# Performance work log

Measured on AMD Instinct MI355X. Metric: run time of the kernel, lower is better.

The kernel has to match this reference:

```python
import jax, jax.numpy as jnp
import numpy as np

HIDDEN = 128
SIGMA_A = 15.0
FACTOR_A = 180.0 / (SIGMA_A * np.pi)  # 180/(sigma_a*pi)


def _sinusoidal_embedding(indices, d_model):
    # torch: omegas = idx.view(-1,1,1)*div_term.view(1,-1,1); cat([sin,cos],dim=2)
    # -> interleaved [sin0, cos0, sin1, cos1, ...]
    div_term = jnp.exp(jnp.arange(0, d_model, 2, dtype=jnp.float32) * (-np.log(10000.0) / d_model))
    omegas = indices[..., None] * div_term  # (*, d/2)
    emb = jnp.stack([jnp.sin(omegas), jnp.cos(omegas)], axis=-1)  # (*, d/2, 2)
    return emb.reshape(*indices.shape, d_model)


def setup_inputs() -> dict:
    key = jax.random.key(0)
    k1, k2, k3 = jax.random.split(key, 3)
    B, N = 1, 1024
    points = jax.random.normal(k1, (B, N, 3), dtype=jnp.float32)
    normals = jax.random.normal(k2, (B, N, 3), dtype=jnp.float32)
    W = jax.random.normal(k3, (HIDDEN, HIDDEN), dtype=jnp.float32) / np.sqrt(HIDDEN)
    b = jnp.zeros((HIDDEN,), dtype=jnp.float32)
    return {"points": points, "normals": normals, "W": W, "b": b}


def reference(points, normals, W, b):
    # pairwise angle between normal_i (ref) and normal_j (anc), k=1 so mean over k is a no-op
    ref = normals[:, :, None, :]   # (B,N,1,3) -> n_i
    anc = normals[:, None, :, :]   # (B,1,N,3) -> n_j
    cross = jnp.cross(ref, anc)                    # (B,N,N,3)
    sin_v = jnp.linalg.norm(cross, axis=-1)        # (B,N,N)
    cos_v = jnp.sum(ref * anc, axis=-1)            # (B,N,N)
    angles = jnp.arctan2(sin_v, cos_v)
    a_indices = angles * FACTOR_A
    a_emb = _sinusoidal_embedding(a_indices, HIDDEN)  # (B,N,N,HIDDEN)
    a_emb = jax.lax.stop_gradient(a_emb)  # torch: no_grad + detach
    return a_emb @ W.T + b                # nn.Linear
```

## Files before the change

### kernel.cpp

```cpp
#include <hip/hip_runtime.h>
#include <hip/hip_bf16.h>
#include <math.h>


#define N_PTS 1024
#define HID   128
#define K_TAB 127
#define A_MAX 12.0f
#define T_OF_ANGLE 40.1070456591f
#define NEG_LOG1E4_OVER_128 (-0.0719557841f)

__global__ __launch_bounds__(128) void build_table(
        const float* __restrict__ W,
        const float* __restrict__ b,
        float* __restrict__ T) {
    __shared__ float ss[64], sc[64];
    const int t = blockIdx.x;
    const float a = (float)t * (A_MAX / (float)(K_TAB - 1));
    const int k = threadIdx.x;
    if (k < 64) {
        float omega = expf((float)(2 * k) * NEG_LOG1E4_OVER_128);
        ss[k] = sinf(a * omega);
        sc[k] = cosf(a * omega);
    }
    __syncthreads();
    float acc = b[k];
    const float* wrow = W + k * HID;
#pragma unroll 8
    for (int m = 0; m < 64; ++m) {
        acc += ss[m] * wrow[2 * m] + sc[m] * wrow[2 * m + 1];
    }
    T[t * HID + k] = acc;
}

__global__ __launch_bounds__(256) void compute_t(
        const float* __restrict__ normals,
        float* __restrict__ tv) {
    const int p = blockIdx.x * 256 + threadIdx.x;
    const int i = p >> 10;
    const int j = p & 1023;
    float ax = normals[3 * i],     ay = normals[3 * i + 1], az = normals[3 * i + 2];
    float bx = normals[3 * j],     by = normals[3 * j + 1], bz = normals[3 * j + 2];
    float cx = ay * bz - az * by;
    float cy = az * bx - ax * bz;
    float cz = ax * by - ay * bx;
    float sv = sqrtf(cx * cx + cy * cy + cz * cz);
    float cv = ax * bx + ay * by + az * bz;
    float ang = atan2f(sv, cv);
    tv[p] = ang * T_OF_ANGLE;
}

__device__ __forceinline__ float4 lerp4(const float* __restrict__ lt,
                                        float t, int lane) {
    int idx = (int)floorf(t);
    idx = idx < 0 ? 0 : (idx > K_TAB - 2 ? K_TAB - 2 : idx);
    float frac = t - (float)idx;
    const float4 v0 = *(const float4*)(lt + idx * HID + lane * 4);
    const float4 v1 = *(const float4*)(lt + idx * HID + HID + lane * 4);
    float4 v;
    v.x = fmaf(frac, v1.x - v0.x, v0.x);
    v.y = fmaf(frac, v1.y - v0.y, v0.y);
    v.z = fmaf(frac, v1.z - v0.z, v0.z);
    v.w = fmaf(frac, v1.w - v0.w, v0.w);
    return v;
}

__global__ __launch_bounds__(256) void lerp_out(
        const float* __restrict__ T,
        const float* __restrict__ tv,
        float* __restrict__ out) {
    __shared__ float lt[K_TAB * HID];
    for (int idx = threadIdx.x; idx < (K_TAB * HID) / 4; idx += 256)
        ((float4*)lt)[idx] = ((const float4*)T)[idx];
    __syncthreads();

    const int lane  = threadIdx.x & 31;
    const int slot  = (blockIdx.x * 256 + threadIdx.x) >> 5;
    const int nslot = (gridDim.x * 256) >> 5;
    const int npair2 = (N_PTS * N_PTS) / 2;

    for (int p2 = slot; p2 < npair2; p2 += nslot) {
        const int p = p2 * 2;
        const float2 tt = *(const float2*)(tv + p);
        float4 v0 = lerp4(lt, tt.x, lane);
        float4 v1 = lerp4(lt, tt.y, lane);
        *(float4*)(out + (size_t)p * HID + lane * 4) = v0;
        *(float4*)(out + ((size_t)p + 1) * HID + lane * 4) = v1;
    }
}

extern "C" void kernel_launch(void* const* d_in, const int* in_sizes, int n_in,
                              void* d_out, int out_size, void* d_ws, size_t ws_size,
                              hipStream_t stream) {
    const float* normals = (const float*)d_in[1];
    const float* W       = (const float*)d_in[2];
    const float* b       = (const float*)d_in[3];
    float* out           = (float*)d_out;

    float* T  = (float*)d_ws;
    float* tv = (float*)((char*)d_ws + 65536);

    build_table<<<K_TAB, 128, 0, stream>>>(W, b, T);
    compute_t<<<(N_PTS * N_PTS) / 256, 256, 0, stream>>>(normals, tv);
    lerp_out<<<1024, 256, 0, stream>>>(T, tv, out);
}
```

Before: 570.5 us.

## Fuse angle computation into table-lerp output kernel with wave shuffles

Removes the separate kernel that wrote per-pair table coordinates to global memory; each 64-lane wave now computes 64 angles and broadcasts them via shuffles while writing output rows. This drops one launch and the intermediate round trip, and repacks work so a full wave writes two rows per step. It adds more per-thread compute (atan2, shuffles) inside the store loop and halves the grid.

After: 523.3 us. 8.3% less time.

```diff
diff --git a/kernel.cpp b/kernel.cpp
--- a/kernel.cpp
+++ b/kernel.cpp
@@ -1,5 +1,4 @@
 #include <hip/hip_runtime.h>
-#include <hip/hip_bf16.h>
 #include <math.h>
 
 
@@ -33,59 +32,51 @@
     T[t * HID + k] = acc;
 }
 
-__global__ __launch_bounds__(256) void compute_t(
+__global__ __launch_bounds__(256) void fused_out(
         const float* __restrict__ normals,
-        float* __restrict__ tv) {
-    const int p = blockIdx.x * 256 + threadIdx.x;
-    const int i = p >> 10;
-    const int j = p & 1023;
-    float ax = normals[3 * i],     ay = normals[3 * i + 1], az = normals[3 * i + 2];
-    float bx = normals[3 * j],     by = normals[3 * j + 1], bz = normals[3 * j + 2];
-    float cx = ay * bz - az * by;
-    float cy = az * bx - ax * bz;
-    float cz = ax * by - ay * bx;
-    float sv = sqrtf(cx * cx + cy * cy + cz * cz);
-    float cv = ax * bx + ay * by + az * bz;
-    float ang = atan2f(sv, cv);
-    tv[p] = ang * T_OF_ANGLE;
-}
-
-__device__ __forceinline__ float4 lerp4(const float* __restrict__ lt,
-                                        float t, int lane) {
-    int idx = (int)floorf(t);
-    idx = idx < 0 ? 0 : (idx > K_TAB - 2 ? K_TAB - 2 : idx);
-    float frac = t - (float)idx;
-    const float4 v0 = *(const float4*)(lt + idx * HID + lane * 4);
-    const float4 v1 = *(const float4*)(lt + idx * HID + HID + lane * 4);
-    float4 v;
-    v.x = fmaf(frac, v1.x - v0.x, v0.x);
-    v.y = fmaf(frac, v1.y - v0.y, v0.y);
-    v.z = fmaf(frac, v1.z - v0.z, v0.z);
-    v.w = fmaf(frac, v1.w - v0.w, v0.w);
-    return v;
-}
-
-__global__ __launch_bounds__(256) void lerp_out(
         const float* __restrict__ T,
-        const float* __restrict__ tv,
         float* __restrict__ out) {
     __shared__ float lt[K_TAB * HID];
     for (int idx = threadIdx.x; idx < (K_TAB * HID) / 4; idx += 256)
         ((float4*)lt)[idx] = ((const float4*)T)[idx];
     __syncthreads();
 
-    const int lane  = threadIdx.x & 31;
-    const int slot  = (blockIdx.x * 256 + threadIdx.x) >> 5;
-    const int nslot = (gridDim.x * 256) >> 5;
-    const int npair2 = (N_PTS * N_PTS) / 2;
+    const int lane = threadIdx.x & 63;
+    const int half = lane >> 5;
+    const int l32  = lane & 31;
+    const int gwave = (blockIdx.x * 256 + threadIdx.x) >> 6;
+    const int nwave = (gridDim.x * 256) >> 6;
 
-    for (int p2 = slot; p2 < npair2; p2 += nslot) {
-        const int p = p2 * 2;
-        const float2 tt = *(const float2*)(tv + p);
-        float4 v0 = lerp4(lt, tt.x, lane);
-        float4 v1 = lerp4(lt, tt.y, lane);
-        *(float4*)(out + (size_t)p * HID + lane * 4) = v0;
-        *(float4*)(out + ((size_t)p + 1) * HID + lane * 4) = v1;
+    for (int base = gwave * 64; base < N_PTS * N_PTS; base += nwave * 64) {
+        const int p = base + lane;
+        const int i = p >> 10;
+        const int j = p & 1023;
+        float ax = normals[3 * i],  ay = normals[3 * i + 1], az = normals[3 * i + 2];
+        float bx = normals[3 * j],  by = normals[3 * j + 1], bz = normals[3 * j + 2];
+        float cx = ay * bz - az * by;
+        float cy = az * bx - ax * bz;
+        float cz = ax * by - ay * bx;
+        float sv = sqrtf(cx * cx + cy * cy + cz * cz);
+        float cv = ax * bx + ay * by + az * bz;
+        float tval = atan2f(sv, cv) * T_OF_ANGLE;
+
+        float* orow = out + (size_t)(base + half) * HID + l32 * 4;
+#pragma unroll 4
+        for (int k = 0; k < 32; ++k) {
+            float t = __shfl(tval, 2 * k + half, 64);
+            int idx = (int)t;
+            idx = idx > K_TAB - 2 ? K_TAB - 2 : idx;
+            float frac = t - (float)idx;
+            const float4 v0 = *(const float4*)(lt + idx * HID + l32 * 4);
+            const float4 v1 = *(const float4*)(lt + idx * HID + HID + l32 * 4);
+            float4 r;
+            r.x = fmaf(frac, v1.x - v0.x, v0.x);
+            r.y = fmaf(frac, v1.y - v0.y, v0.y);
+            r.z = fmaf(frac, v1.z - v0.z, v0.z);
+            r.w = fmaf(frac, v1.w - v0.w, v0.w);
+            *(float4*)orow = r;
+            orow += 2 * HID;
+        }
     }
 }
 
@@ -97,10 +88,8 @@
     const float* b       = (const float*)d_in[3];
     float* out           = (float*)d_out;
 
-    float* T  = (float*)d_ws;
-    float* tv = (float*)((char*)d_ws + 65536);
+    float* T = (float*)d_ws;
 
     build_table<<<K_TAB, 128, 0, stream>>>(W, b, T);
-    compute_t<<<(N_PTS * N_PTS) / 256, 256, 0, stream>>>(normals, tv);
-    lerp_out<<<1024, 256, 0, stream>>>(T, tv, out);
+    fused_out<<<512, 256, 0, stream>>>(normals, T, out);
 }
```
